# Kernel tuning notes

Measured on AMD Instinct MI355X. Metric: run time of the kernel, lower is better.

The kernel has to match this reference:

```python
import jax, jax.numpy as jnp
import numpy as np

D_MODEL = 1024
NUM_HEADS = 16
MAX_SEQ_LEN = 2048
BATCH = 4
SEQ_LEN = 2048


def setup_inputs() -> dict:
    key = jax.random.key(0)
    ks = jax.random.split(key, 7)
    s = 0.02
    return {
        "x": jax.random.normal(ks[0], (BATCH, SEQ_LEN, D_MODEL), dtype=jnp.float32),
        "Wq": jax.random.normal(ks[1], (D_MODEL, D_MODEL), dtype=jnp.float32) * s,
        "Wk": jax.random.normal(ks[2], (D_MODEL, D_MODEL), dtype=jnp.float32) * s,
        "Wv": jax.random.normal(ks[3], (D_MODEL, D_MODEL), dtype=jnp.float32) * s,
        "Wo": jax.random.normal(ks[4], (D_MODEL, D_MODEL), dtype=jnp.float32) * s,
        "bo": jnp.zeros((D_MODEL,), dtype=jnp.float32),
        "bias_table": jax.random.normal(ks[5], (2 * MAX_SEQ_LEN - 1, NUM_HEADS), dtype=jnp.float32) * s,
    }


def reference(x, Wq, Wk, Wv, Wo, bo, bias_table):
    B, S, D = x.shape
    H = NUM_HEADS
    hd = D // H
    scale = hd ** -0.5

    # torch Linear: y = x @ W.T
    q = (x @ Wq.T).reshape(B, S, H, hd).transpose(0, 2, 1, 3)  # [B,H,S,hd]
    k = (x @ Wk.T).reshape(B, S, H, hd).transpose(0, 2, 1, 3)
    v = (x @ Wv.T).reshape(B, S, H, hd).transpose(0, 2, 1, 3)

    scores = jnp.einsum("bhqd,bhkd->bhqk", q, k) * scale  # [B,H,S,S]

    # relative index: coords[:,None] - coords[None,:] + max_seq_len - 1
    coords = jnp.arange(S)
    rel_idx = coords[:, None] - coords[None, :] + MAX_SEQ_LEN - 1  # [S,S]
    rel_bias = bias_table[rel_idx]              # [S,S,H]
    rel_bias = rel_bias.transpose(2, 0, 1)[None]  # [1,H,S,S]

    probs = jax.nn.softmax(scores + rel_bias, axis=-1)
    ctx = jnp.einsum("bhqk,bhkd->bhqd", probs, v)  # [B,H,S,hd]
    ctx = ctx.transpose(0, 2, 1, 3).reshape(B, S, D)
    return ctx @ Wo.T + bo
```

## Files before the change

### kernel.cpp

```cpp
#include <hip/hip_runtime.h>
#include <string.h>

typedef unsigned short u16;
typedef unsigned int   u32;
typedef __attribute__((ext_vector_type(8))) short short8;
typedef __attribute__((ext_vector_type(4))) float f32x4;
typedef __attribute__((ext_vector_type(16))) float f32x16;
typedef __attribute__((ext_vector_type(2))) __fp16 h2;
typedef __attribute__((ext_vector_type(8))) __fp16 h8;
typedef __attribute__((ext_vector_type(2))) unsigned int u32x2;

__device__ __forceinline__ u16 f2b(float f) {
  u32 u = __float_as_uint(f);
  u32 r = (u + 0x7fffu + ((u >> 16) & 1u)) >> 16;
  return (u16)r;
}
__device__ __forceinline__ void cp16(const u16* g, u16* l) {
  __builtin_amdgcn_global_load_lds(
      (const __attribute__((address_space(1))) void*)g,
      (__attribute__((address_space(3))) void*)l, 16, 0, 0);
}
__device__ __forceinline__ void plswap(u32& a, u32& b) {
  u32x2 r = __builtin_amdgcn_permlane32_swap(a, b, false, false);
  a = r[0]; b = r[1];
}

__global__ __launch_bounds__(256) void cvt_f2b_kernel(const float* __restrict__ in,
                                                      u16* __restrict__ out, int n) {
  int i = (blockIdx.x * 256 + threadIdx.x) * 4;
  if (i + 3 < n) {
    float4 v = *(const float4*)&in[i];
    ushort4 o = make_ushort4(f2b(v.x), f2b(v.y), f2b(v.z), f2b(v.w));
    *(ushort4*)&out[i] = o;
  }
}
__global__ __launch_bounds__(256) void cvtw_kernel(const float* __restrict__ w0,
                                                   const float* __restrict__ w1,
                                                   const float* __restrict__ w2,
                                                   const float* __restrict__ w3,
                                                   u16* __restrict__ out) {
  const float* src = (blockIdx.y == 0) ? w0 : (blockIdx.y == 1) ? w1
                   : (blockIdx.y == 2) ? w2 : w3;
  int i = (blockIdx.x * 256 + threadIdx.x) * 4;
  float4 v = *(const float4*)&src[i];
  ushort4 o = make_ushort4(f2b(v.x), f2b(v.y), f2b(v.z), f2b(v.w));
  *(ushort4*)&out[(size_t)blockIdx.y * 1048576 + i] = o;
}

template<int MODE>
__global__ __launch_bounds__(256) void gemm128_bt(
    const u16* __restrict__ A, const u16* __restrict__ Bw,
    void* __restrict__ outp, const float* __restrict__ bias,
    const int M, const int N, const int K) {
  __shared__ __attribute__((aligned(16))) u16 As[2][128 * 32];
  __shared__ __attribute__((aligned(16))) u16 Bs[2][128 * 32];

  const u16* Bw2 = Bw;
  if (MODE == 0) Bw2 += ((size_t)blockIdx.z) << 20;

  const int tid  = threadIdx.x;
  const int wave = tid >> 6, lane = tid & 63;
  const int quad = lane >> 4, l15 = lane & 15;
  const int wm   = (wave >> 1) * 64, wn = (wave & 1) * 64;
  const int m0   = blockIdx.x * 128, n0 = blockIdx.y * 128;

  const int srow = wave * 32 + (lane >> 2);
  const int scol = (lane & 3) * 8;
  const u16* gA0 = A   + (size_t)(m0 + srow) * K + scol;
  const u16* gA1 = gA0 + (size_t)16 * K;
  const u16* gB0 = Bw2 + (size_t)(n0 + srow) * K + scol;
  const u16* gB1 = gB0 + (size_t)16 * K;
  const int lo0 = (wave * 32) * 32, lo1 = (wave * 32 + 16) * 32;

  cp16(gA0, &As[0][lo0]); cp16(gA1, &As[0][lo1]);
  cp16(gB0, &Bs[0][lo0]); cp16(gB1, &Bs[0][lo1]);
  gA0 += 32; gA1 += 32; gB0 += 32; gB1 += 32;

  f32x4 acc[4][4] = {};
  const int nk = K >> 5;
  for (int kt = 0; kt < nk; ++kt) {
    const int cur = kt & 1;
    __syncthreads();
    if (kt + 1 < nk) {
      cp16(gA0, &As[1 - cur][lo0]); cp16(gA1, &As[1 - cur][lo1]);
      cp16(gB0, &Bs[1 - cur][lo0]); cp16(gB1, &Bs[1 - cur][lo1]);
      gA0 += 32; gA1 += 32; gB0 += 32; gB1 += 32;
    }
    short8 af[4], bf[4];
    #pragma unroll
    for (int mi = 0; mi < 4; ++mi)
      af[mi] = *(const short8*)&As[cur][(wm + mi * 16 + l15) * 32 + quad * 8];
    #pragma unroll
    for (int ni = 0; ni < 4; ++ni)
      bf[ni] = *(const short8*)&Bs[cur][(wn + ni * 16 + l15) * 32 + quad * 8];
    #pragma unroll
    for (int mi = 0; mi < 4; ++mi)
      #pragma unroll
      for (int ni = 0; ni < 4; ++ni)
        acc[mi][ni] = __builtin_amdgcn_mfma_f32_16x16x32_bf16(af[mi], bf[ni], acc[mi][ni], 0, 0, 0);
  }

  #pragma unroll
  for (int mi = 0; mi < 4; ++mi)
    #pragma unroll
    for (int ni = 0; ni < 4; ++ni) {
      if (MODE == 0 && blockIdx.z == 2) {
        int mb = m0 + wm + mi * 16 + quad * 4;
        int n  = n0 + wn + ni * 16 + l15;
        int b = mb >> 11, s = mb & 2047, h = n >> 6, d = n & 63;
        u16* out = (u16*)outp + (((size_t)2) << 23);
        h2 p0 = __builtin_amdgcn_cvt_pkrtz(acc[mi][ni][0], acc[mi][ni][1]);
        h2 p1 = __builtin_amdgcn_cvt_pkrtz(acc[mi][ni][2], acc[mi][ni][3]);
        ushort4 o;
        memcpy(&o.x, &p0, 4);
        memcpy(&o.z, &p1, 4);
        *(ushort4*)&out[((((size_t)b * 16 + h) * 64 + d) << 11) + s] = o;
      } else {
        #pragma unroll
        for (int r = 0; r < 4; ++r) {
          int m = m0 + wm + mi * 16 + quad * 4 + r;
          int n = n0 + wn + ni * 16 + l15;
          float v = acc[mi][ni][r];
          if (MODE == 0) {
            int b = m >> 11, s = m & 2047, h = n >> 6, d = n & 63;
            u16* out = (u16*)outp + (((size_t)blockIdx.z) << 23);
            out[((((size_t)b * 16 + h) * 2048 + s) << 6) + d] = f2b(v);
          } else {
            ((float*)outp)[(size_t)m * N + n] = v + bias[n];
          }
        }
      }
    }
}

__global__ __launch_bounds__(256, 2) void attn_mfma_kernel(
    const u16* __restrict__ qb, const u16* __restrict__ kb, const u16* __restrict__ vtb,
    const float* __restrict__ bias_table, u16* __restrict__ ctx) {
  __shared__ __attribute__((aligned(16))) u16 Ks[2][64 * 64];
  __shared__ __attribute__((aligned(16))) u16 Vs[2][64 * 64];
  __shared__ __attribute__((aligned(16))) float bias_s[2304];

  const int tid  = threadIdx.x;
  const int wave = tid >> 6, lane = tid & 63;
  const int l31  = lane & 31, hi = lane >> 5;
  const int xsw  = l31 & 7;
  const int bh   = blockIdx.x, h = bh & 15, b = bh >> 4;
  const int q0   = blockIdx.y * 256;

  for (int i = tid; i < 2303; i += 256)
    bias_s[i] = bias_table[(q0 + i) * 16 + h] * 1.44269504f;

  short8 aQ[2][4];
  #pragma unroll
  for (int qs = 0; qs < 2; ++qs)
    #pragma unroll
    for (int ks = 0; ks < 4; ++ks)
      aQ[qs][ks] = *(const short8*)&qb[((size_t)bh * 2048 + q0 + wave * 64 + qs * 32 + l31) * 64
                                       + ks * 16 + hi * 8];

  f32x16 accO[2][2] = {};
  float  lsum[2] = {0.f, 0.f};

  const int krow = lane >> 3;
  const int kchk = (lane & 7) ^ krow;
  const u16* kbase = kb + (((size_t)bh * 2048) << 6);

  const int srow = tid >> 2, t0 = tid & 3, ssw = srow & 7;
  const u16* vrow = vtb + (((size_t)bh * 64 + srow) << 11) + t0 * 16;
  const int vo0 = srow * 64 + (((2 * t0    ) ^ ssw) << 3);
  const int vo1 = srow * 64 + (((2 * t0 + 1) ^ ssw) << 3);

  short8 vpre0 = *(const short8*)&vrow[0];
  short8 vpre1 = *(const short8*)&vrow[8];
  *(short8*)&Vs[0][vo0] = vpre0;
  *(short8*)&Vs[0][vo1] = vpre1;
  #pragma unroll
  for (int g = 0; g < 2; ++g)
    cp16(kbase + (size_t)(wave * 16 + g * 8 + krow) * 64 + kchk * 8,
         &Ks[0][(wave * 16 + g * 8) * 64]);
  vpre0 = *(const short8*)&vrow[64];
  vpre1 = *(const short8*)&vrow[72];

  for (int kt = 0; kt < 32; ++kt) {
    const int cur = kt & 1;
    __syncthreads();
    if (kt < 31) {
      #pragma unroll
      for (int g = 0; g < 2; ++g)
        cp16(kbase + (size_t)((kt + 1) * 64 + wave * 16 + g * 8 + krow) * 64 + kchk * 8,
             &Ks[1 - cur][(wave * 16 + g * 8) * 64]);
      *(short8*)&Vs[1 - cur][vo0] = vpre0;
      *(short8*)&Vs[1 - cur][vo1] = vpre1;
      if (kt < 30) {
        const u16* vp = vrow + ((size_t)(kt + 2) << 6);
        vpre0 = *(const short8*)&vp[0];
        vpre1 = *(const short8*)&vp[8];
      }
    }

    #pragma unroll
    for (int t = 0; t < 2; ++t) {
      short8 aK[4];
      #pragma unroll
      for (int ks = 0; ks < 4; ++ks)
        aK[ks] = *(const short8*)&Ks[cur][(t * 32 + l31) * 64
                                          + (((ks * 2 + hi) ^ xsw) << 3)];
      f32x16 accS[2] = {};
      #pragma unroll
      for (int ks = 0; ks < 4; ++ks)
        #pragma unroll
        for (int qs = 0; qs < 2; ++qs)
          accS[qs] = __builtin_amdgcn_mfma_f32_32x32x16_bf16(aK[ks], aQ[qs][ks], accS[qs], 0, 0, 0);

      u32 d[2][8];
      #pragma unroll
      for (int qs = 0; qs < 2; ++qs) {
        const int ib = wave * 64 + qs * 32 + l31 - kt * 64 - t * 32 - 4 * hi + 2047;
        #pragma unroll
        for (int rg = 0; rg < 4; ++rg) {
          const int bb = ib - 8 * rg;
          float p0 = __builtin_amdgcn_exp2f(fmaf(accS[qs][4 * rg + 0], 0.18033688f, bias_s[bb    ]));
          float p1 = __builtin_amdgcn_exp2f(fmaf(accS[qs][4 * rg + 1], 0.18033688f, bias_s[bb - 1]));
          float p2 = __builtin_amdgcn_exp2f(fmaf(accS[qs][4 * rg + 2], 0.18033688f, bias_s[bb - 2]));
          float p3 = __builtin_amdgcn_exp2f(fmaf(accS[qs][4 * rg + 3], 0.18033688f, bias_s[bb - 3]));
          lsum[qs] += (p0 + p1) + (p2 + p3);
          h2 e0; e0[0] = (__fp16)p0; e0[1] = (__fp16)p1;
          h2 e1; e1[0] = (__fp16)p2; e1[1] = (__fp16)p3;
          memcpy(&d[qs][2 * rg],     &e0, 4);
          memcpy(&d[qs][2 * rg + 1], &e1, 4);
        }
      }

      #pragma unroll
      for (int sl = 0; sl < 2; ++sl) {
        const int ch = ((t * 2 + sl) * 2 + hi) ^ xsw;
        short8 av0 = *(const short8*)&Vs[cur][(     l31) * 64 + (ch << 3)];
        short8 av1 = *(const short8*)&Vs[cur][(32 + l31) * 64 + (ch << 3)];
        h8 avh0, avh1;
        memcpy(&avh0, &av0, 16);
        memcpy(&avh1, &av1, 16);
        #pragma unroll
        for (int qs = 0; qs < 2; ++qs) {
          u32 F0 = d[qs][4 * sl], F1 = d[qs][4 * sl + 1];
          u32 F2 = d[qs][4 * sl + 2], F3 = d[qs][4 * sl + 3];
          plswap(F0, F2);
          plswap(F1, F3);
          union { u32 w[4]; h8 v; } uf;
          uf.w[0] = F0; uf.w[1] = F1; uf.w[2] = F2; uf.w[3] = F3;
          accO[qs][0] = __builtin_amdgcn_mfma_f32_32x32x16_f16(avh0, uf.v, accO[qs][0], 0, 0, 0);
          accO[qs][1] = __builtin_amdgcn_mfma_f32_32x32x16_f16(avh1, uf.v, accO[qs][1], 0, 0, 0);
        }
      }
    }
  }

  #pragma unroll
  for (int qs = 0; qs < 2; ++qs) {
    const float ltot = lsum[qs] + __shfl_xor(lsum[qs], 32);
    const float inv  = 1.0f / ltot;
    const int q = q0 + wave * 64 + qs * 32 + l31;
    #pragma unroll
    for (int dt = 0; dt < 2; ++dt)
      #pragma unroll
      for (int rg = 0; rg < 4; ++rg) {
        ushort4 o = make_ushort4(f2b(accO[qs][dt][4 * rg + 0] * inv), f2b(accO[qs][dt][4 * rg + 1] * inv),
                                 f2b(accO[qs][dt][4 * rg + 2] * inv), f2b(accO[qs][dt][4 * rg + 3] * inv));
        *(ushort4*)&ctx[((size_t)b * 2048 + q) * 1024 + h * 64 + dt * 32 + rg * 8 + hi * 4] = o;
      }
  }
}

extern "C" void kernel_launch(void* const* d_in, const int* in_sizes, int n_in,
                              void* d_out, int out_size, void* d_ws, size_t ws_size,
                              hipStream_t stream) {
  const float* x          = (const float*)d_in[0];
  const float* Wq         = (const float*)d_in[1];
  const float* Wk         = (const float*)d_in[2];
  const float* Wv         = (const float*)d_in[3];
  const float* Wo         = (const float*)d_in[4];
  const float* bo         = (const float*)d_in[5];
  const float* bias_table = (const float*)d_in[6];
  float* out = (float*)d_out;

  char* ws = (char*)d_ws;
  u16* xb   = (u16*)(ws);
  u16* wqb  = (u16*)(ws + 16777216);
  u16* wob  = (u16*)(ws + 16777216 + 3 * 2097152);
  u16* qb   = (u16*)(ws + 25165824);
  u16* kb   = qb + 8388608;
  u16* vtb  = kb + 8388608;
  u16* ctxb = (u16*)(ws + 75497472);

  cvt_f2b_kernel<<<8192, 256, 0, stream>>>(x, xb, 8388608);
  cvtw_kernel<<<dim3(1024, 4), 256, 0, stream>>>(Wq, Wk, Wv, Wo, wqb);

  gemm128_bt<0><<<dim3(64, 8, 3), 256, 0, stream>>>(
      xb, wqb, (void*)qb, nullptr, 8192, 1024, 1024);

  attn_mfma_kernel<<<dim3(64, 8), 256, 0, stream>>>(qb, kb, vtb, bias_table, ctxb);

  gemm128_bt<1><<<dim3(64, 8), 256, 0, stream>>>(
      ctxb, wob, (void*)out, bo, 8192, 1024, 1024);
}
```

Before: 276.0 us.

## Compute softmax row sums via MFMA, vectorize bias reads, and raise MFMA priority

The softmax denominator is now accumulated by an extra f16 MFMA that multiplies the probability fragment by a ones vector, replacing the per-element VALU adds and the final cross-lane shuffle. The bias table is repacked in LDS as overlapping float4 entries, so each group of four bias values comes from one vector LDS read instead of four scalar reads; Ks is used as scratch during this setup. s_setprio is raised around the MFMA blocks to favour matrix-issue scheduling. The trade-off is more MFMA work in the PV stage and a much larger LDS footprint, which may limit occupancy.

```diff
diff --git a/kernel.cpp b/kernel.cpp
--- a/kernel.cpp
+++ b/kernel.cpp
@@ -138,7 +138,7 @@
     const float* __restrict__ bias_table, u16* __restrict__ ctx) {
   __shared__ __attribute__((aligned(16))) u16 Ks[2][64 * 64];
   __shared__ __attribute__((aligned(16))) u16 Vs[2][64 * 64];
-  __shared__ __attribute__((aligned(16))) float bias_s[2304];
+  __shared__ __attribute__((aligned(16))) f32x4 bias4[2304];
 
   const int tid  = threadIdx.x;
   const int wave = tid >> 6, lane = tid & 63;
@@ -147,8 +147,24 @@
   const int bh   = blockIdx.x, h = bh & 15, b = bh >> 4;
   const int q0   = blockIdx.y * 256;
 
-  for (int i = tid; i < 2303; i += 256)
-    bias_s[i] = bias_table[(q0 + i) * 16 + h] * 1.44269504f;
+  {
+    float* btmp = (float*)&Ks[0][0];
+    for (int i = tid; i < 2304; i += 256) {
+      int j = q0 + i; if (j > 4094) j = 4094;
+      btmp[i] = bias_table[j * 16 + h] * 1.44269504f;
+    }
+    __syncthreads();
+    for (int i = tid; i < 2304; i += 256) {
+      f32x4 v;
+      v[0] = btmp[i];
+      v[1] = btmp[(i + 1) & 2047 ? (i + 1 < 2304 ? i + 1 : 2303) : (i + 1 < 2304 ? i + 1 : 2303)];
+      v[1] = btmp[i + 1 < 2304 ? i + 1 : 2303];
+      v[2] = btmp[i + 2 < 2304 ? i + 2 : 2303];
+      v[3] = btmp[i + 3 < 2304 ? i + 3 : 2303];
+      bias4[i] = v;
+    }
+    __syncthreads();
+  }
 
   short8 aQ[2][4];
   #pragma unroll
@@ -159,7 +175,10 @@
                                        + ks * 16 + hi * 8];
 
   f32x16 accO[2][2] = {};
-  float  lsum[2] = {0.f, 0.f};
+  f32x16 accL[2]    = {};
+
+  const h8 ones8 = {(__fp16)1.f, (__fp16)1.f, (__fp16)1.f, (__fp16)1.f,
+                    (__fp16)1.f, (__fp16)1.f, (__fp16)1.f, (__fp16)1.f};
 
   const int krow = lane >> 3;
   const int kchk = (lane & 7) ^ krow;
@@ -206,24 +225,25 @@
         aK[ks] = *(const short8*)&Ks[cur][(t * 32 + l31) * 64
                                           + (((ks * 2 + hi) ^ xsw) << 3)];
       f32x16 accS[2] = {};
+      __builtin_amdgcn_s_setprio(1);
       #pragma unroll
       for (int ks = 0; ks < 4; ++ks)
         #pragma unroll
         for (int qs = 0; qs < 2; ++qs)
           accS[qs] = __builtin_amdgcn_mfma_f32_32x32x16_bf16(aK[ks], aQ[qs][ks], accS[qs], 0, 0, 0);
+      __builtin_amdgcn_s_setprio(0);
 
       u32 d[2][8];
       #pragma unroll
       for (int qs = 0; qs < 2; ++qs) {
-        const int ib = wave * 64 + qs * 32 + l31 - kt * 64 - t * 32 - 4 * hi + 2047;
+        const int ib3 = wave * 64 + qs * 32 + l31 - kt * 64 - t * 32 - 4 * hi + 2044;
         #pragma unroll
         for (int rg = 0; rg < 4; ++rg) {
-          const int bb = ib - 8 * rg;
-          float p0 = __builtin_amdgcn_exp2f(fmaf(accS[qs][4 * rg + 0], 0.18033688f, bias_s[bb    ]));
-          float p1 = __builtin_amdgcn_exp2f(fmaf(accS[qs][4 * rg + 1], 0.18033688f, bias_s[bb - 1]));
-          float p2 = __builtin_amdgcn_exp2f(fmaf(accS[qs][4 * rg + 2], 0.18033688f, bias_s[bb - 2]));
-          float p3 = __builtin_amdgcn_exp2f(fmaf(accS[qs][4 * rg + 3], 0.18033688f, bias_s[bb - 3]));
-          lsum[qs] += (p0 + p1) + (p2 + p3);
+          const f32x4 bb4 = bias4[ib3 - 8 * rg];
+          float p0 = __builtin_amdgcn_exp2f(fmaf(accS[qs][4 * rg + 0], 0.18033688f, bb4[3]));
+          float p1 = __builtin_amdgcn_exp2f(fmaf(accS[qs][4 * rg + 1], 0.18033688f, bb4[2]));
+          float p2 = __builtin_amdgcn_exp2f(fmaf(accS[qs][4 * rg + 2], 0.18033688f, bb4[1]));
+          float p3 = __builtin_amdgcn_exp2f(fmaf(accS[qs][4 * rg + 3], 0.18033688f, bb4[0]));
           h2 e0; e0[0] = (__fp16)p0; e0[1] = (__fp16)p1;
           h2 e1; e1[0] = (__fp16)p2; e1[1] = (__fp16)p3;
           memcpy(&d[qs][2 * rg],     &e0, 4);
@@ -239,6 +259,7 @@
         h8 avh0, avh1;
         memcpy(&avh0, &av0, 16);
         memcpy(&avh1, &av1, 16);
+        __builtin_amdgcn_s_setprio(1);
         #pragma unroll
         for (int qs = 0; qs < 2; ++qs) {
           u32 F0 = d[qs][4 * sl], F1 = d[qs][4 * sl + 1];
@@ -249,15 +270,16 @@
           uf.w[0] = F0; uf.w[1] = F1; uf.w[2] = F2; uf.w[3] = F3;
           accO[qs][0] = __builtin_amdgcn_mfma_f32_32x32x16_f16(avh0, uf.v, accO[qs][0], 0, 0, 0);
           accO[qs][1] = __builtin_amdgcn_mfma_f32_32x32x16_f16(avh1, uf.v, accO[qs][1], 0, 0, 0);
+          accL[qs]    = __builtin_amdgcn_mfma_f32_32x32x16_f16(ones8, uf.v, accL[qs], 0, 0, 0);
         }
+        __builtin_amdgcn_s_setprio(0);
       }
     }
   }
 
   #pragma unroll
   for (int qs = 0; qs < 2; ++qs) {
-    const float ltot = lsum[qs] + __shfl_xor(lsum[qs], 32);
-    const float inv  = 1.0f / ltot;
+    const float inv = 1.0f / accL[qs][0];
     const int q = q0 + wave * 64 + qs * 32 + l31;
     #pragma unroll
     for (int dt = 0; dt < 2; ++dt)
```

New measurement: 279.9 us. No clear change (+1.4%).
